# Kernel tuning notes

Measured on AMD Instinct MI355X. Metric: run time of the kernel, lower is better.

The kernel has to match this reference:

```python
import jax, jax.numpy as jnp
import numpy as np


def _embed(x, W, b):
    # nn.Linear: x @ W.T + b, then L2 normalize rows (Normalize(power=2), no eps)
    z = x @ W.T + b
    norm = jnp.sqrt(jnp.sum(z * z, axis=1, keepdims=True))
    return z / norm


def setup_inputs() -> dict:
    key = jax.random.key(0)
    ks = jax.random.split(key, 6)
    B, S_DIM, T_DIM, FEAT = 16384, 768, 1024, 128
    return {
        "f_s": jax.random.normal(ks[0], (B, S_DIM), dtype=jnp.float32),
        "f_t": jax.random.normal(ks[1], (B, T_DIM), dtype=jnp.float32),
        "W_s": jax.random.normal(ks[2], (FEAT, S_DIM), dtype=jnp.float32) * 0.02,
        "b_s": jax.random.normal(ks[3], (FEAT,), dtype=jnp.float32) * 0.02,
        "W_t": jax.random.normal(ks[4], (FEAT, T_DIM), dtype=jnp.float32) * 0.02,
        "b_t": jax.random.normal(ks[5], (FEAT,), dtype=jnp.float32) * 0.02,
    }


def reference(f_s, f_t, W_s, b_s, W_t, b_t):
    es = _embed(f_s, W_s, b_s)  # [B, feat]
    et = _embed(f_t, W_t, b_t)  # [B, feat]
    bsz = es.shape[0]
    # diag(es @ et.T) == row-wise dot product; same math, no BxB intermediate
    diag = jnp.sum(es * et, axis=1)  # [B]
    loss = -jnp.sum(diag) / bsz
    return loss.reshape(1)  # matches torch .view(-1,1).sum(0) -> shape [1]
```

## Files before the change

kernel.cpp:

```cpp
#include <hip/hip_runtime.h>
#include <math.h>

typedef __attribute__((ext_vector_type(8))) short bf16x8;
typedef __attribute__((ext_vector_type(8))) unsigned short u16x8;
typedef __attribute__((ext_vector_type(4))) float f32x4;

#define FEAT 128
#define KS   768
#define KT   1024
#define BM   64
#define KB   64
#define LDK  72

__device__ __forceinline__ unsigned short f2bf(float f) {
    unsigned u = __float_as_uint(f);
    u += 0x7fff + ((u >> 16) & 1);
    return (unsigned short)(u >> 16);
}
__device__ __forceinline__ float bf2f(unsigned short h) {
    return __uint_as_float((unsigned)h << 16);
}

__global__ __launch_bounds__(256) void convert_w(
    const float* __restrict__ Ws, const float* __restrict__ Wt,
    unsigned short* __restrict__ WhiS, unsigned short* __restrict__ WloS,
    unsigned short* __restrict__ WhiT, unsigned short* __restrict__ WloT)
{
    const int NS = FEAT * KS;
    int e = blockIdx.x * 256 + threadIdx.x;
    if (e < NS) {
        float w = Ws[e];
        unsigned short h = f2bf(w);
        WhiS[e] = h;
        WloS[e] = f2bf(w - bf2f(h));
    } else {
        int e2 = e - NS;
        float w = Wt[e2];
        unsigned short h = f2bf(w);
        WhiT[e2] = h;
        WloT[e2] = f2bf(w - bf2f(h));
    }
}

__global__ __launch_bounds__(512, 2) void gemm_fused(
    const float* __restrict__ f_s, const float* __restrict__ f_t,
    const unsigned short* __restrict__ WhiS, const unsigned short* __restrict__ WloS,
    const unsigned short* __restrict__ WhiT, const unsigned short* __restrict__ WloT,
    const float* __restrict__ b_s, const float* __restrict__ b_t,
    float* __restrict__ partials)
{
    __shared__ unsigned short sAhi[BM][LDK], sAlo[BM][LDK];
    __shared__ unsigned short sBhi[FEAT][LDK], sBlo[FEAT][LDK];
    __shared__ float sRed[64][4][3];

    const int tid  = threadIdx.x;
    const int lane = tid & 63;
    const int wv   = tid >> 6;
    const int wm   = wv >> 2;
    const int wn   = wv & 3;
    const int l15  = lane & 15;
    const int l4   = lane >> 4;
    const int row0 = blockIdx.x * BM;

    const int arow = tid >> 3;
    const int ak8  = tid & 7;

    f32x4 accS[2][2], accT[2][2];
    #pragma unroll
    for (int m = 0; m < 2; ++m)
        #pragma unroll
        for (int n = 0; n < 2; ++n) {
            accS[m][n] = (f32x4){0.f, 0.f, 0.f, 0.f};
            accT[m][n] = (f32x4){0.f, 0.f, 0.f, 0.f};
        }

    #pragma unroll
    for (int ph = 0; ph < 2; ++ph) {
        const float*          f   = ph ? f_t  : f_s;
        const unsigned short* Whi = ph ? WhiT : WhiS;
        const unsigned short* Wlo = ph ? WloT : WloS;
        const int             K   = ph ? KT   : KS;
        f32x4* acc = ph ? &accT[0][0] : &accS[0][0];

        const float* fbase = f + (size_t)(row0 + arow) * K + ak8 * 8;

        for (int k0 = 0; k0 < K; k0 += KB) {
            float4 a0 = *(const float4*)(fbase + k0);
            float4 a1 = *(const float4*)(fbase + k0 + 4);
            uint4 bh[2], bl[2];
            int brow[2], bk8[2];
            #pragma unroll
            for (int j = 0; j < 2; ++j) {
                int c = j * 512 + tid;
                brow[j] = c >> 3; bk8[j] = c & 7;
                size_t off = (size_t)brow[j] * K + k0 + bk8[j] * 8;
                bh[j] = *(const uint4*)(Whi + off);
                bl[j] = *(const uint4*)(Wlo + off);
            }

            __syncthreads();

            float av[8] = {a0.x, a0.y, a0.z, a0.w, a1.x, a1.y, a1.z, a1.w};
            u16x8 vh, vl;
            #pragma unroll
            for (int i = 0; i < 8; ++i) {
                unsigned short h = f2bf(av[i]);
                vh[i] = h;
                vl[i] = f2bf(av[i] - bf2f(h));
            }
            *(u16x8*)&sAhi[arow][ak8 * 8] = vh;
            *(u16x8*)&sAlo[arow][ak8 * 8] = vl;

            #pragma unroll
            for (int j = 0; j < 2; ++j) {
                *(uint4*)&sBhi[brow[j]][bk8[j] * 8] = bh[j];
                *(uint4*)&sBlo[brow[j]][bk8[j] * 8] = bl[j];
            }

            __syncthreads();

            #pragma unroll
            for (int ks = 0; ks < 2; ++ks) {
                const int ka = ks * 32 + l4 * 8;
                bf16x8 ah[2], al[2], bhf[2], blf[2];
                #pragma unroll
                for (int m = 0; m < 2; ++m) {
                    int r = wm * 32 + m * 16 + l15;
                    ah[m] = *(const bf16x8*)&sAhi[r][ka];
                    al[m] = *(const bf16x8*)&sAlo[r][ka];
                }
                #pragma unroll
                for (int n = 0; n < 2; ++n) {
                    int cn = wn * 32 + n * 16 + l15;
                    bhf[n] = *(const bf16x8*)&sBhi[cn][ka];
                    blf[n] = *(const bf16x8*)&sBlo[cn][ka];
                }
                #pragma unroll
                for (int m = 0; m < 2; ++m)
                    #pragma unroll
                    for (int n = 0; n < 2; ++n) {
                        f32x4 c = acc[m * 2 + n];
                        c = __builtin_amdgcn_mfma_f32_16x16x32_bf16(ah[m], bhf[n], c, 0, 0, 0);
                        c = __builtin_amdgcn_mfma_f32_16x16x32_bf16(ah[m], blf[n], c, 0, 0, 0);
                        c = __builtin_amdgcn_mfma_f32_16x16x32_bf16(al[m], bhf[n], c, 0, 0, 0);
                        acc[m * 2 + n] = c;
                    }
            }
        }
    }

    #pragma unroll
    for (int n = 0; n < 2; ++n) {
        int col = wn * 32 + n * 16 + l15;
        float bsv = b_s[col], btv = b_t[col];
        #pragma unroll
        for (int m = 0; m < 2; ++m) {
            accS[m][n] += bsv;
            accT[m][n] += btv;
        }
    }

    #pragma unroll
    for (int m = 0; m < 2; ++m) {
        #pragma unroll
        for (int r = 0; r < 4; ++r) {
            float s2 = accS[m][0][r] * accS[m][0][r] + accS[m][1][r] * accS[m][1][r];
            float t2 = accT[m][0][r] * accT[m][0][r] + accT[m][1][r] * accT[m][1][r];
            float dt = accS[m][0][r] * accT[m][0][r] + accS[m][1][r] * accT[m][1][r];
            #pragma unroll
            for (int d = 1; d < 16; d <<= 1) {
                s2 += __shfl_xor(s2, d, 64);
                t2 += __shfl_xor(t2, d, 64);
                dt += __shfl_xor(dt, d, 64);
            }
            if (l15 == 0) {
                int row = wm * 32 + m * 16 + l4 * 4 + r;
                sRed[row][wn][0] = s2;
                sRed[row][wn][1] = t2;
                sRed[row][wn][2] = dt;
            }
        }
    }
    __syncthreads();
    if (tid < 64) {
        float s2 = sRed[tid][0][0] + sRed[tid][1][0] + sRed[tid][2][0] + sRed[tid][3][0];
        float t2 = sRed[tid][0][1] + sRed[tid][1][1] + sRed[tid][2][1] + sRed[tid][3][1];
        float dt = sRed[tid][0][2] + sRed[tid][1][2] + sRed[tid][2][2] + sRed[tid][3][2];
        float v = dt / sqrtf(s2 * t2);
        #pragma unroll
        for (int d = 1; d < 64; d <<= 1) v += __shfl_xor(v, d, 64);
        if (tid == 0) partials[blockIdx.x] = v;
    }
}

__global__ __launch_bounds__(256) void finalize(
    const float* __restrict__ partials, float* __restrict__ out)
{
    const int tid = threadIdx.x;
    float v = partials[tid];
    #pragma unroll
    for (int d = 1; d < 64; d <<= 1) v += __shfl_xor(v, d, 64);
    __shared__ float r[4];
    if ((tid & 63) == 0) r[tid >> 6] = v;
    __syncthreads();
    if (tid == 0) out[0] = -(r[0] + r[1] + r[2] + r[3]) / 16384.0f;
}

extern "C" void kernel_launch(void* const* d_in, const int* in_sizes, int n_in,
                              void* d_out, int out_size, void* d_ws, size_t ws_size,
                              hipStream_t stream)
{
    const float* f_s = (const float*)d_in[0];
    const float* f_t = (const float*)d_in[1];
    const float* W_s = (const float*)d_in[2];
    const float* b_s = (const float*)d_in[3];
    const float* W_t = (const float*)d_in[4];
    const float* b_t = (const float*)d_in[5];

    unsigned char* ws = (unsigned char*)d_ws;
    unsigned short* WhiS = (unsigned short*)(ws);
    unsigned short* WloS = (unsigned short*)(ws + 196608);
    unsigned short* WhiT = (unsigned short*)(ws + 393216);
    unsigned short* WloT = (unsigned short*)(ws + 655360);
    float*          part = (float*)(ws + 917504);

    convert_w<<<896, 256, 0, stream>>>(W_s, W_t, WhiS, WloS, WhiT, WloT);
    gemm_fused<<<256, 512, 0, stream>>>(f_s, f_t, WhiS, WloS, WhiT, WloT,
                                        b_s, b_t, part);
    finalize<<<1, 256, 0, stream>>>(part, (float*)d_out);
}
```

Measured before the change: 204.0 us.

## Halve row tile, prefetch next K-tile into registers, XOR-swizzle LDS

Shrinks the per-block row tile from 64 to 32 and launches 512 blocks of 256 threads, so more blocks are resident across the CUs. Global loads for the next K tile are issued before the MFMA work on the current tile, including across the switch from the student to the teacher phase, so memory latency is hidden behind compute. The padded LDS layout is replaced by an XOR swizzle to avoid bank conflicts without padding. In exchange each block reloads the full weight tile for half as many rows, which doubles weight traffic through L2, and the extra prefetch registers raise register pressure.

```diff
diff --git a/kernel.cpp b/kernel.cpp
--- a/kernel.cpp
+++ b/kernel.cpp
@@ -8,9 +8,10 @@
 #define FEAT 128
 #define KS   768
 #define KT   1024
-#define BM   64
+#define BM   32
 #define KB   64
-#define LDK  72
+#define NTS  (KS / KB)
+#define NTT  (KT / KB)
 
 __device__ __forceinline__ unsigned short f2bf(float f) {
     unsigned u = __float_as_uint(f);
@@ -42,28 +43,32 @@
     }
 }
 
-__global__ __launch_bounds__(512, 2) void gemm_fused(
+__global__ __launch_bounds__(256, 2) void gemm_fused(
     const float* __restrict__ f_s, const float* __restrict__ f_t,
     const unsigned short* __restrict__ WhiS, const unsigned short* __restrict__ WloS,
     const unsigned short* __restrict__ WhiT, const unsigned short* __restrict__ WloT,
     const float* __restrict__ b_s, const float* __restrict__ b_t,
     float* __restrict__ partials)
 {
-    __shared__ unsigned short sAhi[BM][LDK], sAlo[BM][LDK];
-    __shared__ unsigned short sBhi[FEAT][LDK], sBlo[FEAT][LDK];
-    __shared__ float sRed[64][4][3];
+    __shared__ unsigned short sAhi[BM][KB],   sAlo[BM][KB];
+    __shared__ unsigned short sBhi[FEAT][KB], sBlo[FEAT][KB];
+    __shared__ float sRed[BM][4][3];
 
     const int tid  = threadIdx.x;
     const int lane = tid & 63;
-    const int wv   = tid >> 6;
-    const int wm   = wv >> 2;
-    const int wn   = wv & 3;
+    const int wn   = tid >> 6;
     const int l15  = lane & 15;
     const int l4   = lane >> 4;
     const int row0 = blockIdx.x * BM;
 
-    const int arow = tid >> 3;
-    const int ak8  = tid & 7;
+    const int arow   = tid >> 3;
+    const int ak8    = tid & 7;
+    const int achunk = ak8 ^ (arow & 7);
+    const int brbase = tid >> 3;
+    const int bk8    = tid & 7;
+
+    float4 a0, a1;
+    uint4  bh[4], bl[4];
 
     f32x4 accS[2][2], accT[2][2];
     #pragma unroll
@@ -74,79 +79,84 @@
             accT[m][n] = (f32x4){0.f, 0.f, 0.f, 0.f};
         }
 
-    #pragma unroll
-    for (int ph = 0; ph < 2; ++ph) {
-        const float*          f   = ph ? f_t  : f_s;
-        const unsigned short* Whi = ph ? WhiT : WhiS;
-        const unsigned short* Wlo = ph ? WloT : WloS;
-        const int             K   = ph ? KT   : KS;
-        f32x4* acc = ph ? &accT[0][0] : &accS[0][0];
-
-        const float* fbase = f + (size_t)(row0 + arow) * K + ak8 * 8;
-
-        for (int k0 = 0; k0 < K; k0 += KB) {
-            float4 a0 = *(const float4*)(fbase + k0);
-            float4 a1 = *(const float4*)(fbase + k0 + 4);
-            uint4 bh[2], bl[2];
-            int brow[2], bk8[2];
-            #pragma unroll
-            for (int j = 0; j < 2; ++j) {
-                int c = j * 512 + tid;
-                brow[j] = c >> 3; bk8[j] = c & 7;
-                size_t off = (size_t)brow[j] * K + k0 + bk8[j] * 8;
-                bh[j] = *(const uint4*)(Whi + off);
-                bl[j] = *(const uint4*)(Wlo + off);
-            }
-
-            __syncthreads();
-
-            float av[8] = {a0.x, a0.y, a0.z, a0.w, a1.x, a1.y, a1.z, a1.w};
-            u16x8 vh, vl;
-            #pragma unroll
-            for (int i = 0; i < 8; ++i) {
-                unsigned short h = f2bf(av[i]);
-                vh[i] = h;
-                vl[i] = f2bf(av[i] - bf2f(h));
-            }
-            *(u16x8*)&sAhi[arow][ak8 * 8] = vh;
-            *(u16x8*)&sAlo[arow][ak8 * 8] = vl;
-
-            #pragma unroll
-            for (int j = 0; j < 2; ++j) {
-                *(uint4*)&sBhi[brow[j]][bk8[j] * 8] = bh[j];
-                *(uint4*)&sBlo[brow[j]][bk8[j] * 8] = bl[j];
-            }
-
-            __syncthreads();
-
-            #pragma unroll
-            for (int ks = 0; ks < 2; ++ks) {
-                const int ka = ks * 32 + l4 * 8;
-                bf16x8 ah[2], al[2], bhf[2], blf[2];
-                #pragma unroll
-                for (int m = 0; m < 2; ++m) {
-                    int r = wm * 32 + m * 16 + l15;
-                    ah[m] = *(const bf16x8*)&sAhi[r][ka];
-                    al[m] = *(const bf16x8*)&sAlo[r][ka];
-                }
-                #pragma unroll
-                for (int n = 0; n < 2; ++n) {
-                    int cn = wn * 32 + n * 16 + l15;
-                    bhf[n] = *(const bf16x8*)&sBhi[cn][ka];
-                    blf[n] = *(const bf16x8*)&sBlo[cn][ka];
-                }
-                #pragma unroll
-                for (int m = 0; m < 2; ++m)
-                    #pragma unroll
-                    for (int n = 0; n < 2; ++n) {
-                        f32x4 c = acc[m * 2 + n];
-                        c = __builtin_amdgcn_mfma_f32_16x16x32_bf16(ah[m], bhf[n], c, 0, 0, 0);
-                        c = __builtin_amdgcn_mfma_f32_16x16x32_bf16(ah[m], blf[n], c, 0, 0, 0);
-                        c = __builtin_amdgcn_mfma_f32_16x16x32_bf16(al[m], bhf[n], c, 0, 0, 0);
-                        acc[m * 2 + n] = c;
-                    }
-            }
-        }
+#define PREFETCH(fptr, Whi, Wlo, K, k0)                                          \
+    {                                                                            \
+        const float* fb = (fptr) + (size_t)(row0 + arow) * (K) + (k0) + ak8 * 8; \
+        a0 = *(const float4*)fb;                                                 \
+        a1 = *(const float4*)(fb + 4);                                           \
+        _Pragma("unroll")                                                        \
+        for (int j = 0; j < 4; ++j) {                                            \
+            size_t off = (size_t)(brbase + j * 32) * (K) + (k0) + bk8 * 8;       \
+            bh[j] = *(const uint4*)((Whi) + off);                                \
+            bl[j] = *(const uint4*)((Wlo) + off);                                \
+        }                                                                        \
+    }
+
+#define STAGE()                                                                  \
+    {                                                                            \
+        float av[8] = {a0.x, a0.y, a0.z, a0.w, a1.x, a1.y, a1.z, a1.w};          \
+        u16x8 vh, vl;                                                            \
+        _Pragma("unroll")                                                        \
+        for (int i = 0; i < 8; ++i) {                                            \
+            unsigned short h = f2bf(av[i]);                                      \
+            vh[i] = h; vl[i] = f2bf(av[i] - bf2f(h));                            \
+        }                                                                        \
+        *(u16x8*)&sAhi[arow][achunk * 8] = vh;                                   \
+        *(u16x8*)&sAlo[arow][achunk * 8] = vl;                                   \
+        _Pragma("unroll")                                                        \
+        for (int j = 0; j < 4; ++j) {                                            \
+            int br = brbase + j * 32;                                            \
+            int bc = (bk8 ^ (br & 7)) * 8;                                       \
+            *(uint4*)&sBhi[br][bc] = bh[j];                                      \
+            *(uint4*)&sBlo[br][bc] = bl[j];                                      \
+        }                                                                        \
+    }
+
+#define MFMA_TILE(acc)                                                           \
+    _Pragma("unroll")                                                            \
+    for (int ks = 0; ks < 2; ++ks) {                                             \
+        bf16x8 fah[2], fal[2], fbh[2], fbl[2];                                   \
+        _Pragma("unroll")                                                        \
+        for (int m = 0; m < 2; ++m) {                                            \
+            int r = m * 16 + l15;                                                \
+            int c = ((ks * 4 + l4) ^ (r & 7)) * 8;                               \
+            fah[m] = *(const bf16x8*)&sAhi[r][c];                                \
+            fal[m] = *(const bf16x8*)&sAlo[r][c];                                \
+        }                                                                        \
+        _Pragma("unroll")                                                        \
+        for (int n = 0; n < 2; ++n) {                                            \
+            int r = wn * 32 + n * 16 + l15;                                      \
+            int c = ((ks * 4 + l4) ^ (r & 7)) * 8;                               \
+            fbh[n] = *(const bf16x8*)&sBhi[r][c];                                \
+            fbl[n] = *(const bf16x8*)&sBlo[r][c];                                \
+        }                                                                        \
+        _Pragma("unroll")                                                        \
+        for (int m = 0; m < 2; ++m)                                              \
+            _Pragma("unroll")                                                    \
+            for (int n = 0; n < 2; ++n) {                                        \
+                f32x4 cc = acc[m][n];                                            \
+                cc = __builtin_amdgcn_mfma_f32_16x16x32_bf16(fah[m], fbh[n], cc, 0, 0, 0); \
+                cc = __builtin_amdgcn_mfma_f32_16x16x32_bf16(fah[m], fbl[n], cc, 0, 0, 0); \
+                cc = __builtin_amdgcn_mfma_f32_16x16x32_bf16(fal[m], fbh[n], cc, 0, 0, 0); \
+                acc[m][n] = cc;                                                  \
+            }                                                                    \
+    }
+
+    PREFETCH(f_s, WhiS, WloS, KS, 0);
+    for (int kt = 0; kt < NTS; ++kt) {
+        __syncthreads();
+        STAGE();
+        __syncthreads();
+        if (kt + 1 < NTS) { PREFETCH(f_s, WhiS, WloS, KS, (kt + 1) * KB); }
+        else              { PREFETCH(f_t, WhiT, WloT, KT, 0); }
+        MFMA_TILE(accS);
+    }
+    for (int kt = 0; kt < NTT; ++kt) {
+        __syncthreads();
+        STAGE();
+        __syncthreads();
+        if (kt + 1 < NTT) { PREFETCH(f_t, WhiT, WloT, KT, (kt + 1) * KB); }
+        MFMA_TILE(accT);
     }
 
     #pragma unroll
@@ -174,7 +184,7 @@
                 dt += __shfl_xor(dt, d, 64);
             }
             if (l15 == 0) {
-                int row = wm * 32 + m * 16 + l4 * 4 + r;
+                int row = m * 16 + l4 * 4 + r;
                 sRed[row][wn][0] = s2;
                 sRed[row][wn][1] = t2;
                 sRed[row][wn][2] = dt;
@@ -182,13 +192,13 @@
         }
     }
     __syncthreads();
-    if (tid < 64) {
+    if (tid < 32) {
         float s2 = sRed[tid][0][0] + sRed[tid][1][0] + sRed[tid][2][0] + sRed[tid][3][0];
         float t2 = sRed[tid][0][1] + sRed[tid][1][1] + sRed[tid][2][1] + sRed[tid][3][1];
         float dt = sRed[tid][0][2] + sRed[tid][1][2] + sRed[tid][2][2] + sRed[tid][3][2];
         float v = dt / sqrtf(s2 * t2);
         #pragma unroll
-        for (int d = 1; d < 64; d <<= 1) v += __shfl_xor(v, d, 64);
+        for (int d = 1; d < 32; d <<= 1) v += __shfl_xor(v, d, 64);
         if (tid == 0) partials[blockIdx.x] = v;
     }
 }
@@ -197,7 +207,7 @@
     const float* __restrict__ partials, float* __restrict__ out)
 {
     const int tid = threadIdx.x;
-    float v = partials[tid];
+    float v = partials[tid] + partials[tid + 256];
     #pragma unroll
     for (int d = 1; d < 64; d <<= 1) v += __shfl_xor(v, d, 64);
     __shared__ float r[4];
@@ -225,7 +235,7 @@
     float*          part = (float*)(ws + 917504);
 
     convert_w<<<896, 256, 0, stream>>>(W_s, W_t, WhiS, WloS, WhiT, WloT);
-    gemm_fused<<<256, 512, 0, stream>>>(f_s, f_t, WhiS, WloS, WhiT, WloT,
+    gemm_fused<<<512, 256, 0, stream>>>(f_s, f_t, WhiS, WloS, WhiT, WloT,
                                         b_s, b_t, part);
     finalize<<<1, 256, 0, stream>>>(part, (float*)d_out);
 }
```

Result: slower. 286.8 us (+40.6%).
